# Performance work log

Measured on AMD Instinct MI355X. Metric: run time of the kernel, lower is better.

Reference implementation:

```python
import jax, jax.numpy as jnp
import numpy as np

B, N, SEQ, KCNN = 4, 8192, 12, 2
S = SEQ - KCNN + 1   # 11
H = 11               # K heads, d = 1
SET = 32             # inducing set size
KF, M = 6, 2
ALPHA = 0.5
WALK = 6             # walk_length 5 + start node


def setup_inputs() -> dict:
    key = jax.random.key(0)
    ks = jax.random.split(key, 14)
    # --- row-stochastic random-walk adjacency (create_random_walk_matrix) ---
    rng = np.random.default_rng(0)
    walk = rng.integers(0, N, size=(N, WALK))
    walk[:, 0] = np.arange(N)                      # start node included in walk
    rw = np.zeros((N, N), np.float32)
    rw[np.repeat(np.arange(N), WALK), walk.reshape(-1)] = 1.0
    rw /= rw.sum(1, keepdims=True)                 # D^-1 @ RW

    def lin(k, o, i):
        return (jax.random.normal(k, (o, i), jnp.float32) / np.sqrt(i))

    return {
        "occ": jax.random.normal(ks[0], (B, N, SEQ), jnp.float32),
        "prc": jax.random.uniform(ks[1], (B, N, SEQ), jnp.float32),
        "rw_adj": jnp.asarray(rw),
        "rw_t_W": lin(ks[2], SEQ, SEQ), "rw_t_b": jnp.zeros((SEQ,), jnp.float32),
        "rw_a_W": lin(ks[3], SEQ, SEQ), "rw_a_b": jnp.zeros((SEQ,), jnp.float32),
        "conv_W": jax.random.normal(ks[4], (KCNN, 2), jnp.float32) * 0.5,
        "conv_b": jnp.zeros((), jnp.float32),
        "ba_I": jax.random.normal(ks[5], (2, SET, H), jnp.float32) * 0.1,   # inducing points, 2 bottles
        "ba_W": jax.random.normal(ks[6], (2, 2, 4, H, H), jnp.float32) / np.sqrt(H),  # [bottle][mab][q,k,v,o]
        "ba_b": jnp.zeros((2, 2, 4, H), jnp.float32),
        "fp_W": jax.random.normal(ks[7], (2, S, S), jnp.float32) / np.sqrt(S),
        "fp_b": jnp.zeros((2, S), jnp.float32),
        "tcn_W": jax.random.normal(ks[8], (2, 2, M, M, 3), jnp.float32) / np.sqrt(3 * M),  # [block][conv1/2]
        "tcn_b": jnp.zeros((2, 2, M), jnp.float32),
        "fc1_W": lin(ks[9], KF, S - 1), "fc1_b": jnp.zeros((KF,), jnp.float32),
        "fc2_W": lin(ks[10], M, KF), "fc2_b": jnp.zeros((M,), jnp.float32),
        "fc3_W": lin(ks[11], 1, KF + M), "fc3_b": jnp.zeros((1,), jnp.float32),
    }


def _linear(x, W, b):
    return x @ W.T + b


def _mab(Q, Kin, W, b):
    # Q: (b,Sq,11); Kin: (b,Sk,11); H=11 heads of dim d=1 (scale = 1)
    q = jax.nn.relu(_linear(Q, W[0], b[0]))
    k = jax.nn.relu(_linear(Kin, W[1], b[1]))
    v = jax.nn.relu(_linear(Kin, W[2], b[2]))
    scores = jnp.einsum('bqh,bkh->bhqk', q, k)        # d=1 -> /sqrt(1)
    attn = jax.nn.softmax(scores, axis=-1)
    out = jnp.einsum('bhqk,bkh->bqh', attn, v)
    out = jax.nn.relu(_linear(out, W[3], b[3]))
    # torch cat-of-splits ordering: (H*b, 1, Sq, Sk)
    aw = attn.transpose(1, 0, 2, 3).reshape(H * Q.shape[0], 1, Q.shape[1], Kin.shape[1])
    return out, aw


def _bottle(X, I, W, b):
    # X: (b,n,11), I: (SET,11), W: (2,4,11,11)
    Ib = jnp.broadcast_to(I, (X.shape[0],) + I.shape)
    Hs, aw0 = _mab(Ib, X, W[0], b[0])     # (b,SET,11)
    out, aw1 = _mab(X, Hs, W[1], b[1])    # (b,n,11)
    return out, aw0, aw1


def _causal_conv1d(x, W, b, dilation):
    # x: (N,C,L), W: (O,I,K); left-pad = conv + chomp in torch
    K = W.shape[-1]
    y = jax.lax.conv_general_dilated(x, W, (1,), [((K - 1) * dilation, 0)],
                                     rhs_dilation=(dilation,),
                                     dimension_numbers=('NCH', 'OIH', 'NCH'))
    return y + b[None, :, None]


def reference(occ, prc, rw_adj, rw_t_W, rw_t_b, rw_a_W, rw_a_b, conv_W, conv_b,
              ba_I, ba_W, ba_b, fp_W, fp_b, tcn_W, tcn_b,
              fc1_W, fc1_b, fc2_W, fc2_b, fc3_W, fc3_b):
    b, n, s = occ.shape

    def enhance(x, mult):
        rw = jnp.einsum('ij,bjs->bis', rw_adj, x)     # random-walk propagation
        att = jax.nn.sigmoid(_linear(rw, rw_a_W, rw_a_b))
        tr = _linear(rw, rw_t_W, rw_t_b)
        return x * (1.0 + att * tr) if mult else x + att * tr

    occ_e = enhance(occ, False)
    prc_e = enhance(prc, True)
    data = jnp.stack([occ_e, prc_e], axis=3).reshape(b * n, s, 2)   # (bn,12,2)
    # conv2d (1->1, kernel (2,2)) fused manually -> (bn, 11)
    h = (conv_W[0, 0] * data[:, :-1, 0] + conv_W[0, 1] * data[:, :-1, 1]
         + conv_W[1, 0] * data[:, 1:, 0] + conv_W[1, 1] * data[:, 1:, 1] + conv_b)
    h_conv = h.reshape(b, n, S)

    h1, aw01, aw11 = _bottle(h_conv, ba_I[0], ba_W[0], ba_b[0])
    z1 = jax.nn.leaky_relu(_linear(h1, fp_W[0], fp_b[0]))           # dropout = eval identity
    h2, aw02, aw12 = _bottle(z1, ba_I[1], ba_W[1], ba_b[1])
    z2 = jax.nn.leaky_relu(_linear(h2, fp_W[1], fp_b[1]))

    inner = (1.0 - ALPHA) * z1 + ALPHA * h_conv
    outer = (1.0 - ALPHA) * z2 + ALPHA * inner

    x1 = outer.reshape(b * n, S)
    x = jnp.stack([x1, x1], axis=1)                                 # (bn, 2, S)
    for i in range(2):                                              # TCN blocks, dilations 1,2
        dil = 2 ** i
        o = jax.nn.relu(_causal_conv1d(x, tcn_W[i, 0], tcn_b[i, 0], dil))
        o = jax.nn.relu(_causal_conv1d(o, tcn_W[i, 1], tcn_b[i, 1], dil))
        x = jax.nn.relu(o + x)                                      # residual (no downsample: m==m)
    tcn_out = x.transpose(0, 2, 1)                                  # (bn, S, 2)

    ht = tcn_out[:, -1, :]                                          # (bn, 2)
    hw = tcn_out[:, :-1, :].transpose(0, 2, 1)                      # (bn, 2, S-1)
    Hc = _linear(hw, fc1_W, fc1_b)                                  # (bn, 2, 6)
    Hn = _linear(Hc, fc2_W, fc2_b)                                  # (bn, 2, 2)
    a = jax.nn.sigmoid(jnp.einsum('bij,bj->bi', Hn, ht))            # (bn, 2)
    vt = jnp.einsum('bi,bik->bk', a, Hc)                            # (bn, 6)
    hx = jnp.concatenate([vt, ht], axis=1)                          # (bn, 8)
    y = _linear(hx, fc3_W, fc3_b).reshape(b, n)
    return y, aw01, aw11, aw02, aw12
```

## Files before the change

### kernel.cpp

```cpp
#include <hip/hip_runtime.h>

#define NN 8192
#define BB 4
#define SS 11
#define HHH 11
#define SETQ 32

typedef unsigned long long u64;
typedef float f4 __attribute__((ext_vector_type(4)));

__device__ __forceinline__ float relu_(float x){ return x > 0.f ? x : 0.f; }
__device__ __forceinline__ float lrelu_(float x){ return x > 0.f ? x : 0.01f*x; }
__device__ __forceinline__ float sigm_(float x){ return 1.f/(1.f + __expf(-x)); }

__global__ void k_extract(const float* __restrict__ rw, int* __restrict__ cnt,
                          int* __restrict__ cols, float* __restrict__ vals) {
  int wave = (blockIdx.x * blockDim.x + threadIdx.x) >> 6;
  int lane = threadIdx.x & 63;
  if (wave >= NN) return;
  const float* row = rw + (size_t)wave * NN;
  int base = 0;
  #pragma unroll 1
  for (int g = 0; g < 8; ++g) {
    const float* p = row + g*1024 + lane*4;
    f4 v0 = __builtin_nontemporal_load((const f4*)(p));
    f4 v1 = __builtin_nontemporal_load((const f4*)(p + 256));
    f4 v2 = __builtin_nontemporal_load((const f4*)(p + 512));
    f4 v3 = __builtin_nontemporal_load((const f4*)(p + 768));
    bool a0 = (v0.x!=0.f)|(v0.y!=0.f)|(v0.z!=0.f)|(v0.w!=0.f);
    bool a1 = (v1.x!=0.f)|(v1.y!=0.f)|(v1.z!=0.f)|(v1.w!=0.f);
    bool a2 = (v2.x!=0.f)|(v2.y!=0.f)|(v2.z!=0.f)|(v2.w!=0.f);
    bool a3 = (v3.x!=0.f)|(v3.y!=0.f)|(v3.z!=0.f)|(v3.w!=0.f);
    if (__ballot(a0|a1|a2|a3) != 0ull) {
      f4 vv[4] = {v0, v1, v2, v3};
      bool aa[4] = {a0, a1, a2, a3};
      #pragma unroll
      for (int c = 0; c < 4; ++c) {
        if (__ballot(aa[c]) == 0ull) continue;
        #pragma unroll
        for (int e = 0; e < 4; ++e) {
          float x = vv[c][e];
          u64 m = __ballot(x != 0.0f);
          if (x != 0.0f) {
            int pos = base + __popcll(m & ((1ull << lane) - 1ull));
            if (pos < 6) {
              cols[wave*6 + pos] = g*1024 + c*256 + lane*4 + e;
              vals[wave*6 + pos] = x;
            }
          }
          base += __popcll(m);
        }
      }
      if (base >= 6) break;
    }
  }
  if (lane == 0) cnt[wave] = base > 6 ? 6 : base;
}

__global__ void k_enh_kv(const float* __restrict__ occ, const float* __restrict__ prc,
                         const int* __restrict__ cnt, const int* __restrict__ cols,
                         const float* __restrict__ vals,
                         const float* __restrict__ aW, const float* __restrict__ ab,
                         const float* __restrict__ tW, const float* __restrict__ tb,
                         const float* __restrict__ cW, const float* __restrict__ cb,
                         const float* __restrict__ Wk, const float* __restrict__ bk,
                         const float* __restrict__ Wv, const float* __restrict__ bv,
                         float* __restrict__ h_conv,
                         float* __restrict__ kT, float* __restrict__ vT) {
  __shared__ float s_aW[144], s_tW[144], s_ab[12], s_tb[12];
  __shared__ float sWk[121], sWv[121], sbk[11], sbv[11];
  int t = threadIdx.x;
  for (int l = t; l < 144; l += 128) { s_aW[l] = aW[l]; s_tW[l] = tW[l]; }
  for (int l = t; l < 121; l += 128) { sWk[l] = Wk[l]; sWv[l] = Wv[l]; }
  if (t < 12) { s_ab[t] = ab[t]; s_tb[t] = tb[t]; }
  if (t < 11) { sbk[t] = bk[t]; sbv[t] = bv[t]; }
  __syncthreads();
  int idx = blockIdx.x * 128 + t;
  int b = idx >> 13, i = idx & (NN-1);
  int c = cnt[i];
  int col[6]; float w[6];
  #pragma unroll
  for (int tt = 0; tt < 6; ++tt) {
    col[tt] = tt < c ? cols[i*6+tt] : 0;
    w[tt]   = tt < c ? vals[i*6+tt] : 0.f;
  }
  float rwo[12], rwp[12];
  #pragma unroll
  for (int s = 0; s < 12; ++s) { rwo[s] = 0.f; rwp[s] = 0.f; }
  #pragma unroll
  for (int tt = 0; tt < 6; ++tt) {
    const f4* po = (const f4*)(occ + ((size_t)b*NN + col[tt])*12);
    const f4* pp = (const f4*)(prc + ((size_t)b*NN + col[tt])*12);
    float ww = w[tt];
    #pragma unroll
    for (int s4 = 0; s4 < 3; ++s4) {
      f4 vo = po[s4], vp_ = pp[s4];
      #pragma unroll
      for (int e = 0; e < 4; ++e) { rwo[s4*4+e] += ww*vo[e]; rwp[s4*4+e] += ww*vp_[e]; }
    }
  }
  const f4* xo4 = (const f4*)(occ + (size_t)idx*12);
  const f4* xp4 = (const f4*)(prc + (size_t)idx*12);
  float xo[12], xp[12];
  #pragma unroll
  for (int s4 = 0; s4 < 3; ++s4) {
    f4 vo = xo4[s4], vp_ = xp4[s4];
    #pragma unroll
    for (int e = 0; e < 4; ++e) { xo[s4*4+e] = vo[e]; xp[s4*4+e] = vp_[e]; }
  }
  float oe[12], pe[12];
  #pragma unroll
  for (int s = 0; s < 12; ++s) {
    float atO = s_ab[s], trO = s_tb[s], atP = s_ab[s], trP = s_tb[s];
    #pragma unroll
    for (int u = 0; u < 12; ++u) {
      atO += rwo[u]*s_aW[s*12+u]; trO += rwo[u]*s_tW[s*12+u];
      atP += rwp[u]*s_aW[s*12+u]; trP += rwp[u]*s_tW[s*12+u];
    }
    oe[s] = xo[s] + sigm_(atO)*trO;
    pe[s] = xp[s]*(1.f + sigm_(atP)*trP);
  }
  float c00 = cW[0], c01 = cW[1], c10 = cW[2], c11 = cW[3], cbv = cb[0];
  float h[SS];
  #pragma unroll
  for (int s = 0; s < SS; ++s) {
    h[s] = c00*oe[s] + c01*pe[s] + c10*oe[s+1] + c11*pe[s+1] + cbv;
    h_conv[(size_t)idx*SS + s] = h[s];
  }
  #pragma unroll
  for (int hh = 0; hh < HHH; ++hh) {
    float kk = sbk[hh], vv = sbv[hh];
    #pragma unroll
    for (int u = 0; u < HHH; ++u) { kk += h[u]*sWk[hh*HHH+u]; vv += h[u]*sWv[hh*HHH+u]; }
    kT[((size_t)(b*HHH + hh))*NN + i] = relu_(kk);
    vT[((size_t)(b*HHH + hh))*NN + i] = relu_(vv);
  }
}

__global__ void k_mab0(const float* __restrict__ kT, const float* __restrict__ vT,
                       const float* __restrict__ I, const float* __restrict__ W0,
                       const float* __restrict__ b0, float* __restrict__ aw,
                       float* __restrict__ out0) {
  __shared__ float sm[4], ss[4], sa[4];
  int bid = blockIdx.x;
  int q = bid & 31;
  int h = (bid >> 5) % HHH;
  int b = bid / (32*HHH);
  int t = threadIdx.x;
  int lane = t & 63, wid = t >> 6;
  float qv = b0[h];
  #pragma unroll
  for (int u = 0; u < HHH; ++u) qv += I[q*HHH+u]*W0[h*HHH+u];
  qv = relu_(qv);
  const f4* kp = (const f4*)(kT + ((size_t)(b*HHH + h))*NN);
  const f4* vp = (const f4*)(vT + ((size_t)(b*HHH + h))*NN);
  f4 sc[8];
  #pragma unroll
  for (int kk = 0; kk < 8; ++kk) sc[kk] = qv * kp[t + kk*256];
  float m = -3.0e38f;
  #pragma unroll
  for (int kk = 0; kk < 8; ++kk)
    m = fmaxf(m, fmaxf(fmaxf(sc[kk].x, sc[kk].y), fmaxf(sc[kk].z, sc[kk].w)));
  #pragma unroll
  for (int off = 1; off < 64; off <<= 1) m = fmaxf(m, __shfl_xor(m, off));
  if (lane == 0) sm[wid] = m;
  __syncthreads();
  float M = fmaxf(fmaxf(sm[0], sm[1]), fmaxf(sm[2], sm[3]));
  float s = 0.f;
  #pragma unroll
  for (int kk = 0; kk < 8; ++kk) {
    f4 e;
    e.x = __expf(sc[kk].x - M); e.y = __expf(sc[kk].y - M);
    e.z = __expf(sc[kk].z - M); e.w = __expf(sc[kk].w - M);
    sc[kk] = e;
    s += e.x + e.y + e.z + e.w;
  }
  #pragma unroll
  for (int off = 1; off < 64; off <<= 1) s += __shfl_xor(s, off);
  if (lane == 0) ss[wid] = s;
  __syncthreads();
  float rinv = 1.f / (ss[0] + ss[1] + ss[2] + ss[3]);
  f4* ap = (f4*)(aw + ((size_t)((h*BB + b)*SETQ + q))*NN);
  f4 acc4 = {0.f, 0.f, 0.f, 0.f};
  #pragma unroll
  for (int kk = 0; kk < 8; ++kk) {
    f4 a = sc[kk] * rinv;
    __builtin_nontemporal_store(a, ap + t + kk*256);
    acc4 += a * vp[t + kk*256];
  }
  float acc = acc4.x + acc4.y + acc4.z + acc4.w;
  #pragma unroll
  for (int off = 1; off < 64; off <<= 1) acc += __shfl_xor(acc, off);
  if (lane == 0) sa[wid] = acc;
  __syncthreads();
  if (t == 0) out0[(b*SETQ + q)*HHH + h] = sa[0]+sa[1]+sa[2]+sa[3];
}

template<int FIN>
__global__ void k_mab1(const float* __restrict__ X, const float* __restrict__ out0,
                       const float* __restrict__ W, const float* __restrict__ bbp,
                       const float* __restrict__ fpW, const float* __restrict__ fpb,
                       float* __restrict__ aw, float* __restrict__ zout,
                       float* __restrict__ kT2, float* __restrict__ vT2,
                       const float* __restrict__ Wk2, const float* __restrict__ bk2,
                       const float* __restrict__ Wv2, const float* __restrict__ bv2,
                       const float* __restrict__ hc_,
                       const float* __restrict__ tW, const float* __restrict__ tb,
                       const float* __restrict__ f1W, const float* __restrict__ f1b,
                       const float* __restrict__ f2W, const float* __restrict__ f2b,
                       const float* __restrict__ f3W, const float* __restrict__ f3b,
                       float* __restrict__ y) {
  __shared__ float sHs[352], sk[352], sv[352];
  __shared__ float sX[96], sz[96], souts[96];
  __shared__ float sW3[121], sW10[121], sW11[121], sW12[121], sW13[121], sfW[121];
  __shared__ float sWk2[121], sWv2[121];
  __shared__ float sb3[11], sb10[11], sb11[11], sb12[11], sb13[11], sfb[11], sbk2[11], sbv2[11];
  int t = threadIdx.x;
  int blk = blockIdx.x;
  int vb = (blk & 7)*512 + (blk >> 3);
  int r0 = vb * 8;
  int b = r0 >> 13;
  int i0 = r0 & (NN-1);
  if (t < 121) {
    sW3[t] = W[363+t]; sW10[t] = W[484+t]; sW11[t] = W[484+121+t];
    sW12[t] = W[484+242+t]; sW13[t] = W[484+363+t]; sfW[t] = fpW[t];
    if (!FIN) { sWk2[t] = Wk2[t]; sWv2[t] = Wv2[t]; }
  }
  if (t < 11) {
    sb3[t] = bbp[33+t]; sb10[t] = bbp[44+t]; sb11[t] = bbp[55+t];
    sb12[t] = bbp[66+t]; sb13[t] = bbp[77+t]; sfb[t] = fpb[t];
    if (!FIN) { sbk2[t] = bk2[t]; sbv2[t] = bv2[t]; }
  }
  if (t < 88) sX[t] = X[(size_t)r0*SS + t];
  __syncthreads();
  for (int l = t; l < 352; l += 256) {
    int j = l / 11, hh = l - j*11;
    const float* o = out0 + (b*SETQ + j)*HHH;
    float acc = sb3[hh];
    #pragma unroll
    for (int u = 0; u < HHH; ++u) acc += o[u]*sW3[hh*HHH+u];
    sHs[l] = relu_(acc);
  }
  __syncthreads();
  for (int l = t; l < 352; l += 256) {
    int j = l / 11, hh = l - j*11;
    float a1 = sb11[hh], a2 = sb12[hh];
    #pragma unroll
    for (int u = 0; u < HHH; ++u) { float xx = sHs[j*11+u]; a1 += xx*sW11[hh*HHH+u]; a2 += xx*sW12[hh*HHH+u]; }
    sk[l] = relu_(a1); sv[l] = relu_(a2);
  }
  __syncthreads();
  int wv = t >> 6, lane = t & 63;
  int r = lane >> 3, jg = lane & 7;
  for (int h = wv; h < HHH; h += 4) {
    float qv = sb10[h];
    #pragma unroll
    for (int u = 0; u < HHH; ++u) qv += sX[r*11+u]*sW10[h*HHH+u];
    qv = relu_(qv);
    float sc[4];
    #pragma unroll
    for (int jj = 0; jj < 4; ++jj) sc[jj] = qv*sk[(jg*4+jj)*11 + h];
    float m = fmaxf(fmaxf(sc[0], sc[1]), fmaxf(sc[2], sc[3]));
    m = fmaxf(m, __shfl_xor(m, 1));
    m = fmaxf(m, __shfl_xor(m, 2));
    m = fmaxf(m, __shfl_xor(m, 4));
    float e[4]; float ssum = 0.f;
    #pragma unroll
    for (int jj = 0; jj < 4; ++jj) { e[jj] = __expf(sc[jj]-m); ssum += e[jj]; }
    ssum += __shfl_xor(ssum, 1);
    ssum += __shfl_xor(ssum, 2);
    ssum += __shfl_xor(ssum, 4);
    float rinv = 1.f/ssum;
    f4 av; av.x = e[0]*rinv; av.y = e[1]*rinv; av.z = e[2]*rinv; av.w = e[3]*rinv;
    __builtin_nontemporal_store(av,
        (f4*)(aw + ((size_t)((h*BB + b)*NN + i0 + r))*SETQ + jg*4));
    float acc = av.x*sv[(jg*4+0)*11+h] + av.y*sv[(jg*4+1)*11+h]
              + av.z*sv[(jg*4+2)*11+h] + av.w*sv[(jg*4+3)*11+h];
    acc += __shfl_xor(acc, 1);
    acc += __shfl_xor(acc, 2);
    acc += __shfl_xor(acc, 4);
    if (jg == 0) souts[r*12 + h] = acc;
  }
  __syncthreads();
  if (t < 8) {
    int idx = r0 + t;
    float outm[HHH];
    #pragma unroll
    for (int u = 0; u < HHH; ++u) outm[u] = souts[t*12+u];
    float h1[HHH];
    #pragma unroll
    for (int hh = 0; hh < HHH; ++hh) {
      float acc = sb13[hh];
      #pragma unroll
      for (int u = 0; u < HHH; ++u) acc += outm[u]*sW13[hh*HHH+u];
      h1[hh] = relu_(acc);
    }
    float z[SS];
    #pragma unroll
    for (int s = 0; s < SS; ++s) {
      float acc = sfb[s];
      #pragma unroll
      for (int u = 0; u < SS; ++u) acc += h1[u]*sfW[s*SS+u];
      z[s] = lrelu_(acc);
    }
    if (!FIN) {
      #pragma unroll
      for (int s = 0; s < SS; ++s) {
        zout[(size_t)idx*SS + s] = z[s];
        sz[t*12 + s] = z[s];
      }
    } else {
      float xc[2][SS];
      #pragma unroll
      for (int s = 0; s < SS; ++s) {
        float hv = hc_[(size_t)idx*SS+s];
        float inner = 0.5f*sX[t*11+s] + 0.5f*hv;
        float outer = 0.5f*z[s] + 0.5f*inner;
        xc[0][s] = outer; xc[1][s] = outer;
      }
      #pragma unroll
      for (int blk2 = 0; blk2 < 2; ++blk2) {
        const int dil = 1 << blk2;
        float o1[2][SS], o2[2][SS];
        #pragma unroll
        for (int co = 0; co < 2; ++co) {
          const float* w0 = tW + (((blk2*2+0)*2+co)*2+0)*3;
          const float* w1 = tW + (((blk2*2+0)*2+co)*2+1)*3;
          float bb0 = tb[(blk2*2+0)*2+co];
          #pragma unroll
          for (int tp = 0; tp < SS; ++tp) {
            float acc = bb0 + w0[2]*xc[0][tp] + w1[2]*xc[1][tp];
            if (tp >= dil)   acc += w0[1]*xc[0][tp-dil] + w1[1]*xc[1][tp-dil];
            if (tp >= 2*dil) acc += w0[0]*xc[0][tp-2*dil] + w1[0]*xc[1][tp-2*dil];
            o1[co][tp] = relu_(acc);
          }
        }
        #pragma unroll
        for (int co = 0; co < 2; ++co) {
          const float* w0 = tW + (((blk2*2+1)*2+co)*2+0)*3;
          const float* w1 = tW + (((blk2*2+1)*2+co)*2+1)*3;
          float bb1 = tb[(blk2*2+1)*2+co];
          #pragma unroll
          for (int tp = 0; tp < SS; ++tp) {
            float acc = bb1 + w0[2]*o1[0][tp] + w1[2]*o1[1][tp];
            if (tp >= dil)   acc += w0[1]*o1[0][tp-dil] + w1[1]*o1[1][tp-dil];
            if (tp >= 2*dil) acc += w0[0]*o1[0][tp-2*dil] + w1[0]*o1[1][tp-2*dil];
            o2[co][tp] = relu_(acc);
          }
        }
        #pragma unroll
        for (int co = 0; co < 2; ++co)
          #pragma unroll
          for (int tp = 0; tp < SS; ++tp)
            xc[co][tp] = relu_(o2[co][tp] + xc[co][tp]);
      }
      float ht0 = xc[0][SS-1], ht1 = xc[1][SS-1];
      float Hc[2][6];
      #pragma unroll
      for (int c = 0; c < 2; ++c)
        #pragma unroll
        for (int f = 0; f < 6; ++f) {
          float acc = f1b[f];
          #pragma unroll
          for (int tt = 0; tt < 10; ++tt) acc += xc[c][tt]*f1W[f*10+tt];
          Hc[c][f] = acc;
        }
      float av2[2];
      #pragma unroll
      for (int c = 0; c < 2; ++c) {
        float hn0 = f2b[0], hn1 = f2b[1];
        #pragma unroll
        for (int f = 0; f < 6; ++f) { hn0 += Hc[c][f]*f2W[0*6+f]; hn1 += Hc[c][f]*f2W[1*6+f]; }
        av2[c] = sigm_(hn0*ht0 + hn1*ht1);
      }
      float yv = f3b[0];
      #pragma unroll
      for (int f = 0; f < 6; ++f) yv += f3W[f]*(av2[0]*Hc[0][f] + av2[1]*Hc[1][f]);
      yv += f3W[6]*ht0 + f3W[7]*ht1;
      y[idx] = yv;
    }
  }
  if (!FIN) {
    __syncthreads();
    if (t < 88) {
      int r = t / 11, hh = t - r*11;
      float kk = sbk2[hh], vv = sbv2[hh];
      #pragma unroll
      for (int u = 0; u < HHH; ++u) { float zz = sz[r*12+u]; kk += zz*sWk2[hh*HHH+u]; vv += zz*sWv2[hh*HHH+u]; }
      kT2[((size_t)(b*HHH + hh))*NN + i0 + r] = relu_(kk);
      vT2[((size_t)(b*HHH + hh))*NN + i0 + r] = relu_(vv);
    }
  }
}

extern "C" void kernel_launch(void* const* d_in, const int* in_sizes, int n_in,
                              void* d_out, int out_size, void* d_ws, size_t ws_size,
                              hipStream_t stream) {
  const float* occ    = (const float*)d_in[0];
  const float* prc    = (const float*)d_in[1];
  const float* rw_adj = (const float*)d_in[2];
  const float* rw_t_W = (const float*)d_in[3];
  const float* rw_t_b = (const float*)d_in[4];
  const float* rw_a_W = (const float*)d_in[5];
  const float* rw_a_b = (const float*)d_in[6];
  const float* conv_W = (const float*)d_in[7];
  const float* conv_b = (const float*)d_in[8];
  const float* ba_I   = (const float*)d_in[9];
  const float* ba_W   = (const float*)d_in[10];
  const float* ba_b   = (const float*)d_in[11];
  const float* fp_W   = (const float*)d_in[12];
  const float* fp_b   = (const float*)d_in[13];
  const float* tcn_W  = (const float*)d_in[14];
  const float* tcn_b  = (const float*)d_in[15];
  const float* fc1_W  = (const float*)d_in[16];
  const float* fc1_b  = (const float*)d_in[17];
  const float* fc2_W  = (const float*)d_in[18];
  const float* fc2_b  = (const float*)d_in[19];
  const float* fc3_W  = (const float*)d_in[20];
  const float* fc3_b  = (const float*)d_in[21];

  float* ws = (float*)d_ws;
  int* cnt    = (int*)ws;
  int* cols   = (int*)(ws + 8192);
  float* vals = ws + 57344;
  float* h_conv = ws + 106496;
  float* kT   = ws + 466944;
  float* vT   = ws + 827392;
  float* z1   = ws + 1187840;
  float* kT2  = ws + 1548288;
  float* vT2  = ws + 1908736;
  float* out0  = ws + 2269184;
  float* out0b = ws + 2270592;

  float* out = (float*)d_out;
  float* y    = out;
  float* aw01 = out + 32768;
  float* aw11 = out + 11567104;
  float* aw02 = out + 23101440;
  float* aw12 = out + 34635776;

  const float* W0  = ba_W;
  const float* bb0 = ba_b;
  const float* W1  = ba_W + 968;
  const float* bb1 = ba_b + 88;

  k_extract<<<2048, 256, 0, stream>>>(rw_adj, cnt, cols, vals);
  k_enh_kv<<<256, 128, 0, stream>>>(occ, prc, cnt, cols, vals,
                                    rw_a_W, rw_a_b, rw_t_W, rw_t_b,
                                    conv_W, conv_b,
                                    W0 + 121, bb0 + 11, W0 + 242, bb0 + 22,
                                    h_conv, kT, vT);
  k_mab0<<<BB*HHH*SETQ, 256, 0, stream>>>(kT, vT, ba_I, W0, bb0, aw01, out0);
  k_mab1<0><<<4096, 256, 0, stream>>>(h_conv, out0, W0, bb0, fp_W, fp_b,
                                      aw11, z1, kT2, vT2,
                                      W1 + 121, bb1 + 11, W1 + 242, bb1 + 22,
                                      nullptr, nullptr, nullptr,
                                      nullptr, nullptr, nullptr, nullptr,
                                      nullptr, nullptr, nullptr);
  k_mab0<<<BB*HHH*SETQ, 256, 0, stream>>>(kT2, vT2, ba_I + SETQ*HHH, W1, bb1, aw02, out0b);
  k_mab1<1><<<4096, 256, 0, stream>>>(z1, out0b, W1, bb1, fp_W + 121, fp_b + 11,
                                      aw12, nullptr, nullptr, nullptr,
                                      nullptr, nullptr, nullptr, nullptr,
                                      h_conv,
                                      tcn_W, tcn_b, fc1_W, fc1_b,
                                      fc2_W, fc2_b, fc3_W, fc3_b, y);
}
```

Baseline: 155.3 us.

## Scan adjacency with grid-stride flat loads and atomic row slot insertion

Replaces the per-row wave scan of the dense 8192x8192 adjacency with a flat grid-stride scan over the whole matrix. Each thread handles four float4 loads per iteration and inserts nonzeros through an atomicAdd on a per-row counter, which is zeroed by a new kernel. Because atomics leave entries in arbitrary order, the consumer clamps the count and insertion-sorts the columns. The early break once six nonzeros are found is gone, so every row is read in full, where before most rows could stop early.

```diff
diff --git a/kernel.cpp b/kernel.cpp
--- a/kernel.cpp
+++ b/kernel.cpp
@@ -13,48 +13,43 @@
 __device__ __forceinline__ float lrelu_(float x){ return x > 0.f ? x : 0.01f*x; }
 __device__ __forceinline__ float sigm_(float x){ return 1.f/(1.f + __expf(-x)); }
 
-__global__ void k_extract(const float* __restrict__ rw, int* __restrict__ cnt,
-                          int* __restrict__ cols, float* __restrict__ vals) {
-  int wave = (blockIdx.x * blockDim.x + threadIdx.x) >> 6;
-  int lane = threadIdx.x & 63;
-  if (wave >= NN) return;
-  const float* row = rw + (size_t)wave * NN;
-  int base = 0;
+__global__ void k_zero(int* __restrict__ cnt) {
+  cnt[blockIdx.x * 256 + threadIdx.x] = 0;
+}
+
+__global__ __launch_bounds__(256) void k_extract(
+    const float* __restrict__ rw, int* __restrict__ cnt,
+    int* __restrict__ cols, float* __restrict__ vals) {
+  const size_t NF4 = (size_t)NN * NN / 4;
+  const size_t stride = (size_t)2048 * 256;
+  size_t tid = (size_t)blockIdx.x * 256 + threadIdx.x;
   #pragma unroll 1
-  for (int g = 0; g < 8; ++g) {
-    const float* p = row + g*1024 + lane*4;
-    f4 v0 = __builtin_nontemporal_load((const f4*)(p));
-    f4 v1 = __builtin_nontemporal_load((const f4*)(p + 256));
-    f4 v2 = __builtin_nontemporal_load((const f4*)(p + 512));
-    f4 v3 = __builtin_nontemporal_load((const f4*)(p + 768));
-    bool a0 = (v0.x!=0.f)|(v0.y!=0.f)|(v0.z!=0.f)|(v0.w!=0.f);
-    bool a1 = (v1.x!=0.f)|(v1.y!=0.f)|(v1.z!=0.f)|(v1.w!=0.f);
-    bool a2 = (v2.x!=0.f)|(v2.y!=0.f)|(v2.z!=0.f)|(v2.w!=0.f);
-    bool a3 = (v3.x!=0.f)|(v3.y!=0.f)|(v3.z!=0.f)|(v3.w!=0.f);
-    if (__ballot(a0|a1|a2|a3) != 0ull) {
-      f4 vv[4] = {v0, v1, v2, v3};
-      bool aa[4] = {a0, a1, a2, a3};
-      #pragma unroll
-      for (int c = 0; c < 4; ++c) {
-        if (__ballot(aa[c]) == 0ull) continue;
+  for (size_t i0 = tid; i0 < NF4; i0 += 4*stride) {
+    const size_t i1 = i0 + stride, i2 = i0 + 2*stride, i3 = i0 + 3*stride;
+    f4 v0 = *((const f4*)rw + i0);
+    f4 v1 = *((const f4*)rw + i1);
+    f4 v2 = *((const f4*)rw + i2);
+    f4 v3 = *((const f4*)rw + i3);
+    f4 vv[4] = {v0, v1, v2, v3};
+    size_t ii[4] = {i0, i1, i2, i3};
+    #pragma unroll
+    for (int g = 0; g < 4; ++g) {
+      f4 v = vv[g];
+      if ((v.x!=0.f)|(v.y!=0.f)|(v.z!=0.f)|(v.w!=0.f)) {
+        size_t base = ii[g] * 4;
         #pragma unroll
         for (int e = 0; e < 4; ++e) {
-          float x = vv[c][e];
-          u64 m = __ballot(x != 0.0f);
-          if (x != 0.0f) {
-            int pos = base + __popcll(m & ((1ull << lane) - 1ull));
-            if (pos < 6) {
-              cols[wave*6 + pos] = g*1024 + c*256 + lane*4 + e;
-              vals[wave*6 + pos] = x;
-            }
+          float x = v[e];
+          if (x != 0.f) {
+            int r = (int)((base + e) >> 13);
+            int c = (int)((base + e) & (NN-1));
+            int pos = atomicAdd(&cnt[r], 1);
+            if (pos < 6) { cols[r*6 + pos] = c; vals[r*6 + pos] = x; }
           }
-          base += __popcll(m);
         }
       }
-      if (base >= 6) break;
-    }
-  }
-  if (lane == 0) cnt[wave] = base > 6 ? 6 : base;
+    }
+  }
 }
 
 __global__ void k_enh_kv(const float* __restrict__ occ, const float* __restrict__ prc,
@@ -77,12 +72,18 @@
   __syncthreads();
   int idx = blockIdx.x * 128 + t;
   int b = idx >> 13, i = idx & (NN-1);
-  int c = cnt[i];
+  int c = cnt[i]; c = c > 6 ? 6 : c;
   int col[6]; float w[6];
   #pragma unroll
   for (int tt = 0; tt < 6; ++tt) {
     col[tt] = tt < c ? cols[i*6+tt] : 0;
     w[tt]   = tt < c ? vals[i*6+tt] : 0.f;
+  }
+  for (int a = 1; a < c; ++a) {
+    int cc = col[a]; float vv = w[a];
+    int b2 = a - 1;
+    while (b2 >= 0 && col[b2] > cc) { col[b2+1] = col[b2]; w[b2+1] = w[b2]; --b2; }
+    col[b2+1] = cc; w[b2+1] = vv;
   }
   float rwo[12], rwp[12];
   #pragma unroll
@@ -250,36 +251,38 @@
     sk[l] = relu_(a1); sv[l] = relu_(a2);
   }
   __syncthreads();
-  int wv = t >> 6, lane = t & 63;
-  int r = lane >> 3, jg = lane & 7;
-  for (int h = wv; h < HHH; h += 4) {
-    float qv = sb10[h];
-    #pragma unroll
-    for (int u = 0; u < HHH; ++u) qv += sX[r*11+u]*sW10[h*HHH+u];
-    qv = relu_(qv);
-    float sc[4];
-    #pragma unroll
-    for (int jj = 0; jj < 4; ++jj) sc[jj] = qv*sk[(jg*4+jj)*11 + h];
-    float m = fmaxf(fmaxf(sc[0], sc[1]), fmaxf(sc[2], sc[3]));
-    m = fmaxf(m, __shfl_xor(m, 1));
-    m = fmaxf(m, __shfl_xor(m, 2));
-    m = fmaxf(m, __shfl_xor(m, 4));
-    float e[4]; float ssum = 0.f;
-    #pragma unroll
-    for (int jj = 0; jj < 4; ++jj) { e[jj] = __expf(sc[jj]-m); ssum += e[jj]; }
-    ssum += __shfl_xor(ssum, 1);
-    ssum += __shfl_xor(ssum, 2);
-    ssum += __shfl_xor(ssum, 4);
-    float rinv = 1.f/ssum;
-    f4 av; av.x = e[0]*rinv; av.y = e[1]*rinv; av.z = e[2]*rinv; av.w = e[3]*rinv;
-    __builtin_nontemporal_store(av,
-        (f4*)(aw + ((size_t)((h*BB + b)*NN + i0 + r))*SETQ + jg*4));
-    float acc = av.x*sv[(jg*4+0)*11+h] + av.y*sv[(jg*4+1)*11+h]
-              + av.z*sv[(jg*4+2)*11+h] + av.w*sv[(jg*4+3)*11+h];
-    acc += __shfl_xor(acc, 1);
-    acc += __shfl_xor(acc, 2);
-    acc += __shfl_xor(acc, 4);
-    if (jg == 0) souts[r*12 + h] = acc;
+  {
+    int wv = t >> 6, lane = t & 63;
+    int r = lane >> 3, jg = lane & 7;
+    for (int h = wv; h < HHH; h += 4) {
+      float qv = sb10[h];
+      #pragma unroll
+      for (int u = 0; u < HHH; ++u) qv += sX[r*11+u]*sW10[h*HHH+u];
+      qv = relu_(qv);
+      float sc[4];
+      #pragma unroll
+      for (int jj = 0; jj < 4; ++jj) sc[jj] = qv*sk[(jg*4+jj)*11 + h];
+      float m = fmaxf(fmaxf(sc[0], sc[1]), fmaxf(sc[2], sc[3]));
+      m = fmaxf(m, __shfl_xor(m, 1));
+      m = fmaxf(m, __shfl_xor(m, 2));
+      m = fmaxf(m, __shfl_xor(m, 4));
+      float e[4]; float ssum = 0.f;
+      #pragma unroll
+      for (int jj = 0; jj < 4; ++jj) { e[jj] = __expf(sc[jj]-m); ssum += e[jj]; }
+      ssum += __shfl_xor(ssum, 1);
+      ssum += __shfl_xor(ssum, 2);
+      ssum += __shfl_xor(ssum, 4);
+      float rinv = 1.f/ssum;
+      f4 av; av.x = e[0]*rinv; av.y = e[1]*rinv; av.z = e[2]*rinv; av.w = e[3]*rinv;
+      __builtin_nontemporal_store(av,
+          (f4*)(aw + ((size_t)((h*BB + b)*NN + i0 + r))*SETQ + jg*4));
+      float acc = av.x*sv[(jg*4+0)*11+h] + av.y*sv[(jg*4+1)*11+h]
+                + av.z*sv[(jg*4+2)*11+h] + av.w*sv[(jg*4+3)*11+h];
+      acc += __shfl_xor(acc, 1);
+      acc += __shfl_xor(acc, 2);
+      acc += __shfl_xor(acc, 4);
+      if (jg == 0) souts[r*12 + h] = acc;
+    }
   }
   __syncthreads();
   if (t < 8) {
@@ -429,7 +432,7 @@
   float* z1   = ws + 1187840;
   float* kT2  = ws + 1548288;
   float* vT2  = ws + 1908736;
-  float* out0  = ws + 2269184;
+  float* out0a = ws + 2269184;
   float* out0b = ws + 2270592;
 
   float* out = (float*)d_out;
@@ -444,14 +447,15 @@
   const float* W1  = ba_W + 968;
   const float* bb1 = ba_b + 88;
 
+  k_zero<<<32, 256, 0, stream>>>(cnt);
   k_extract<<<2048, 256, 0, stream>>>(rw_adj, cnt, cols, vals);
   k_enh_kv<<<256, 128, 0, stream>>>(occ, prc, cnt, cols, vals,
                                     rw_a_W, rw_a_b, rw_t_W, rw_t_b,
                                     conv_W, conv_b,
                                     W0 + 121, bb0 + 11, W0 + 242, bb0 + 22,
                                     h_conv, kT, vT);
-  k_mab0<<<BB*HHH*SETQ, 256, 0, stream>>>(kT, vT, ba_I, W0, bb0, aw01, out0);
-  k_mab1<0><<<4096, 256, 0, stream>>>(h_conv, out0, W0, bb0, fp_W, fp_b,
+  k_mab0<<<BB*HHH*SETQ, 256, 0, stream>>>(kT, vT, ba_I, W0, bb0, aw01, out0a);
+  k_mab1<0><<<4096, 256, 0, stream>>>(h_conv, out0a, W0, bb0, fp_W, fp_b,
                                       aw11, z1, kT2, vT2,
                                       W1 + 121, bb1 + 11, W1 + 242, bb1 + 22,
                                       nullptr, nullptr, nullptr,
```

New measurement: 166.4 us. 7.2% more time.

## Process 32 rows per k_mab1 block and widen k_extract loads

Applied to the files above, without the earlier changes.

k_mab1 now handles 32 nodes per block instead of 8, cutting the grid from 4096 to 1024 blocks. This amortizes the per-block setup (weight staging, recomputing inducing-point K/V projections) over four times as many rows. The tail stage now uses 32 threads instead of 8, and the block-index swizzle is adjusted to match. k_extract loads 8 float4 vectors per iteration instead of 4, and uses plain loads instead of nontemporal ones, to get more memory parallelism while scanning the adjacency matrix; the cost is more registers and less parallelism per block.

```diff
diff --git a/kernel.cpp b/kernel.cpp
--- a/kernel.cpp
+++ b/kernel.cpp
@@ -13,29 +13,38 @@
 __device__ __forceinline__ float lrelu_(float x){ return x > 0.f ? x : 0.01f*x; }
 __device__ __forceinline__ float sigm_(float x){ return 1.f/(1.f + __expf(-x)); }
 
-__global__ void k_extract(const float* __restrict__ rw, int* __restrict__ cnt,
-                          int* __restrict__ cols, float* __restrict__ vals) {
+__global__ __launch_bounds__(256) void k_extract(
+    const float* __restrict__ rw, int* __restrict__ cnt,
+    int* __restrict__ cols, float* __restrict__ vals) {
   int wave = (blockIdx.x * blockDim.x + threadIdx.x) >> 6;
   int lane = threadIdx.x & 63;
   if (wave >= NN) return;
   const float* row = rw + (size_t)wave * NN;
   int base = 0;
   #pragma unroll 1
-  for (int g = 0; g < 8; ++g) {
-    const float* p = row + g*1024 + lane*4;
-    f4 v0 = __builtin_nontemporal_load((const f4*)(p));
-    f4 v1 = __builtin_nontemporal_load((const f4*)(p + 256));
-    f4 v2 = __builtin_nontemporal_load((const f4*)(p + 512));
-    f4 v3 = __builtin_nontemporal_load((const f4*)(p + 768));
+  for (int g = 0; g < 4; ++g) {
+    const float* p = row + g*2048 + lane*4;
+    f4 v0 = *(const f4*)(p);
+    f4 v1 = *(const f4*)(p + 256);
+    f4 v2 = *(const f4*)(p + 512);
+    f4 v3 = *(const f4*)(p + 768);
+    f4 v4 = *(const f4*)(p + 1024);
+    f4 v5 = *(const f4*)(p + 1280);
+    f4 v6 = *(const f4*)(p + 1536);
+    f4 v7 = *(const f4*)(p + 1792);
     bool a0 = (v0.x!=0.f)|(v0.y!=0.f)|(v0.z!=0.f)|(v0.w!=0.f);
     bool a1 = (v1.x!=0.f)|(v1.y!=0.f)|(v1.z!=0.f)|(v1.w!=0.f);
     bool a2 = (v2.x!=0.f)|(v2.y!=0.f)|(v2.z!=0.f)|(v2.w!=0.f);
     bool a3 = (v3.x!=0.f)|(v3.y!=0.f)|(v3.z!=0.f)|(v3.w!=0.f);
-    if (__ballot(a0|a1|a2|a3) != 0ull) {
-      f4 vv[4] = {v0, v1, v2, v3};
-      bool aa[4] = {a0, a1, a2, a3};
-      #pragma unroll
-      for (int c = 0; c < 4; ++c) {
+    bool a4 = (v4.x!=0.f)|(v4.y!=0.f)|(v4.z!=0.f)|(v4.w!=0.f);
+    bool a5 = (v5.x!=0.f)|(v5.y!=0.f)|(v5.z!=0.f)|(v5.w!=0.f);
+    bool a6 = (v6.x!=0.f)|(v6.y!=0.f)|(v6.z!=0.f)|(v6.w!=0.f);
+    bool a7 = (v7.x!=0.f)|(v7.y!=0.f)|(v7.z!=0.f)|(v7.w!=0.f);
+    if (__ballot(a0|a1|a2|a3|a4|a5|a6|a7) != 0ull) {
+      f4 vv[8] = {v0, v1, v2, v3, v4, v5, v6, v7};
+      bool aa[8] = {a0, a1, a2, a3, a4, a5, a6, a7};
+      #pragma unroll
+      for (int c = 0; c < 8; ++c) {
         if (__ballot(aa[c]) == 0ull) continue;
         #pragma unroll
         for (int e = 0; e < 4; ++e) {
@@ -44,7 +53,7 @@
           if (x != 0.0f) {
             int pos = base + __popcll(m & ((1ull << lane) - 1ull));
             if (pos < 6) {
-              cols[wave*6 + pos] = g*1024 + c*256 + lane*4 + e;
+              cols[wave*6 + pos] = g*2048 + c*256 + lane*4 + e;
               vals[wave*6 + pos] = x;
             }
           }
@@ -211,14 +220,14 @@
                        const float* __restrict__ f3W, const float* __restrict__ f3b,
                        float* __restrict__ y) {
   __shared__ float sHs[352], sk[352], sv[352];
-  __shared__ float sX[96], sz[96], souts[96];
+  __shared__ float sX[352], sz[384], souts[384];
   __shared__ float sW3[121], sW10[121], sW11[121], sW12[121], sW13[121], sfW[121];
   __shared__ float sWk2[121], sWv2[121];
   __shared__ float sb3[11], sb10[11], sb11[11], sb12[11], sb13[11], sfb[11], sbk2[11], sbv2[11];
   int t = threadIdx.x;
   int blk = blockIdx.x;
-  int vb = (blk & 7)*512 + (blk >> 3);
-  int r0 = vb * 8;
+  int vb = (blk & 7)*128 + (blk >> 3);
+  int r0 = vb * 32;
   int b = r0 >> 13;
   int i0 = r0 & (NN-1);
   if (t < 121) {
@@ -231,7 +240,7 @@
     sb12[t] = bbp[66+t]; sb13[t] = bbp[77+t]; sfb[t] = fpb[t];
     if (!FIN) { sbk2[t] = bk2[t]; sbv2[t] = bv2[t]; }
   }
-  if (t < 88) sX[t] = X[(size_t)r0*SS + t];
+  for (int l = t; l < 352; l += 256) sX[l] = X[(size_t)r0*SS + l];
   __syncthreads();
   for (int l = t; l < 352; l += 256) {
     int j = l / 11, hh = l - j*11;
@@ -250,39 +259,45 @@
     sk[l] = relu_(a1); sv[l] = relu_(a2);
   }
   __syncthreads();
-  int wv = t >> 6, lane = t & 63;
-  int r = lane >> 3, jg = lane & 7;
-  for (int h = wv; h < HHH; h += 4) {
-    float qv = sb10[h];
-    #pragma unroll
-    for (int u = 0; u < HHH; ++u) qv += sX[r*11+u]*sW10[h*HHH+u];
-    qv = relu_(qv);
-    float sc[4];
-    #pragma unroll
-    for (int jj = 0; jj < 4; ++jj) sc[jj] = qv*sk[(jg*4+jj)*11 + h];
-    float m = fmaxf(fmaxf(sc[0], sc[1]), fmaxf(sc[2], sc[3]));
-    m = fmaxf(m, __shfl_xor(m, 1));
-    m = fmaxf(m, __shfl_xor(m, 2));
-    m = fmaxf(m, __shfl_xor(m, 4));
-    float e[4]; float ssum = 0.f;
-    #pragma unroll
-    for (int jj = 0; jj < 4; ++jj) { e[jj] = __expf(sc[jj]-m); ssum += e[jj]; }
-    ssum += __shfl_xor(ssum, 1);
-    ssum += __shfl_xor(ssum, 2);
-    ssum += __shfl_xor(ssum, 4);
-    float rinv = 1.f/ssum;
-    f4 av; av.x = e[0]*rinv; av.y = e[1]*rinv; av.z = e[2]*rinv; av.w = e[3]*rinv;
-    __builtin_nontemporal_store(av,
-        (f4*)(aw + ((size_t)((h*BB + b)*NN + i0 + r))*SETQ + jg*4));
-    float acc = av.x*sv[(jg*4+0)*11+h] + av.y*sv[(jg*4+1)*11+h]
-              + av.z*sv[(jg*4+2)*11+h] + av.w*sv[(jg*4+3)*11+h];
-    acc += __shfl_xor(acc, 1);
-    acc += __shfl_xor(acc, 2);
-    acc += __shfl_xor(acc, 4);
-    if (jg == 0) souts[r*12 + h] = acc;
-  }
-  __syncthreads();
-  if (t < 8) {
+  {
+    int wv = t >> 6, lane = t & 63;
+    int rl = lane >> 3, jg = lane & 7;
+    for (int h = wv; h < HHH; h += 4) {
+      #pragma unroll
+      for (int rg = 0; rg < 4; ++rg) {
+        int r = rg*8 + rl;
+        float qv = sb10[h];
+        #pragma unroll
+        for (int u = 0; u < HHH; ++u) qv += sX[r*11+u]*sW10[h*HHH+u];
+        qv = relu_(qv);
+        float sc[4];
+        #pragma unroll
+        for (int jj = 0; jj < 4; ++jj) sc[jj] = qv*sk[(jg*4+jj)*11 + h];
+        float m = fmaxf(fmaxf(sc[0], sc[1]), fmaxf(sc[2], sc[3]));
+        m = fmaxf(m, __shfl_xor(m, 1));
+        m = fmaxf(m, __shfl_xor(m, 2));
+        m = fmaxf(m, __shfl_xor(m, 4));
+        float e[4]; float ssum = 0.f;
+        #pragma unroll
+        for (int jj = 0; jj < 4; ++jj) { e[jj] = __expf(sc[jj]-m); ssum += e[jj]; }
+        ssum += __shfl_xor(ssum, 1);
+        ssum += __shfl_xor(ssum, 2);
+        ssum += __shfl_xor(ssum, 4);
+        float rinv = 1.f/ssum;
+        f4 av; av.x = e[0]*rinv; av.y = e[1]*rinv; av.z = e[2]*rinv; av.w = e[3]*rinv;
+        __builtin_nontemporal_store(av,
+            (f4*)(aw + ((size_t)((h*BB + b)*NN + i0 + r))*SETQ + jg*4));
+        float acc = av.x*sv[(jg*4+0)*11+h] + av.y*sv[(jg*4+1)*11+h]
+                  + av.z*sv[(jg*4+2)*11+h] + av.w*sv[(jg*4+3)*11+h];
+        acc += __shfl_xor(acc, 1);
+        acc += __shfl_xor(acc, 2);
+        acc += __shfl_xor(acc, 4);
+        if (jg == 0) souts[r*12 + h] = acc;
+      }
+    }
+  }
+  __syncthreads();
+  if (t < 32) {
     int idx = r0 + t;
     float outm[HHH];
     #pragma unroll
@@ -382,8 +397,8 @@
   }
   if (!FIN) {
     __syncthreads();
-    if (t < 88) {
-      int r = t / 11, hh = t - r*11;
+    for (int l = t; l < 352; l += 256) {
+      int r = l / 11, hh = l - r*11;
       float kk = sbk2[hh], vv = sbv2[hh];
       #pragma unroll
       for (int u = 0; u < HHH; ++u) { float zz = sz[r*12+u]; kk += zz*sWk2[hh*HHH+u]; vv += zz*sWv2[hh*HHH+u]; }
@@ -429,7 +444,7 @@
   float* z1   = ws + 1187840;
   float* kT2  = ws + 1548288;
   float* vT2  = ws + 1908736;
-  float* out0  = ws + 2269184;
+  float* out0a = ws + 2269184;
   float* out0b = ws + 2270592;
 
   float* out = (float*)d_out;
@@ -450,15 +465,15 @@
                                     conv_W, conv_b,
                                     W0 + 121, bb0 + 11, W0 + 242, bb0 + 22,
                                     h_conv, kT, vT);
-  k_mab0<<<BB*HHH*SETQ, 256, 0, stream>>>(kT, vT, ba_I, W0, bb0, aw01, out0);
-  k_mab1<0><<<4096, 256, 0, stream>>>(h_conv, out0, W0, bb0, fp_W, fp_b,
+  k_mab0<<<BB*HHH*SETQ, 256, 0, stream>>>(kT, vT, ba_I, W0, bb0, aw01, out0a);
+  k_mab1<0><<<1024, 256, 0, stream>>>(h_conv, out0a, W0, bb0, fp_W, fp_b,
                                       aw11, z1, kT2, vT2,
                                       W1 + 121, bb1 + 11, W1 + 242, bb1 + 22,
                                       nullptr, nullptr, nullptr,
                                       nullptr, nullptr, nullptr, nullptr,
                                       nullptr, nullptr, nullptr);
   k_mab0<<<BB*HHH*SETQ, 256, 0, stream>>>(kT2, vT2, ba_I + SETQ*HHH, W1, bb1, aw02, out0b);
-  k_mab1<1><<<4096, 256, 0, stream>>>(z1, out0b, W1, bb1, fp_W + 121, fp_b + 11,
+  k_mab1<1><<<1024, 256, 0, stream>>>(z1, out0b, W1, bb1, fp_W + 121, fp_b + 11,
                                       aw12, nullptr, nullptr, nullptr,
                                       nullptr, nullptr, nullptr, nullptr,
                                       h_conv,
```

Measured after the change: 126.1 us. 1.23x faster.
